# Optimization experiments

Hardware: AMD Instinct MI355X
Metric: run time of the kernel (lower is better)

## Reference

```python
import jax, jax.numpy as jnp
import numpy as np

B, S, H, E, V = 256, 512, 512, 512, 50257
ENC = 2 * H  # bidirectional encoder feature dim
EPS = 1e-40


def setup_inputs() -> dict:
    key = jax.random.key(0)
    ks = jax.random.split(key, 10)
    return {
        "x": jax.random.normal(ks[0], (B, H), jnp.float32),
        "input_embed": jax.random.normal(ks[1], (B, E), jnp.float32),
        "hidden_state": jax.random.normal(ks[2], (B, H), jnp.float32),
        "encoder_output": jax.random.normal(ks[3], (S, B, ENC), jnp.float32),
        "attn_weights": jax.random.uniform(ks[4], (B, S), jnp.float32),
        "input_ids": jax.random.randint(ks[5], (B, S), 0, V, jnp.int64),
        "proj_w": jax.random.normal(ks[6], (V, H), jnp.float32) * (1.0 / np.sqrt(H)),
        "proj_b": jnp.zeros((V,), jnp.float32),
        "pgen_w": jax.random.normal(ks[7], (1, 3 * H + E), jnp.float32) * (1.0 / np.sqrt(3 * H + E)),
        "pgen_b": jnp.zeros((1,), jnp.float32),
    }


def reference(x, input_embed, hidden_state, encoder_output, attn_weights,
              input_ids, proj_w, proj_b, pgen_w, pgen_b):
    temp = 1.0
    # logit: [B, V]
    logit = x @ proj_w.T + proj_b
    # context_state: sum_s attn[b,s] * enc[s,b,:] -> [B, ENC]
    context_state = jnp.einsum("bs,sbh->bh", attn_weights, encoder_output)
    feat = jnp.concatenate([hidden_state, input_embed, context_state], axis=1)
    p_gen = jax.nn.sigmoid(feat @ pgen_w.T + pgen_b)  # [B, 1]
    vocab_dist = jax.nn.softmax(logit / temp, axis=1)
    vocab_dist_ = p_gen * vocab_dist
    p_attn_dist = (1.0 - p_gen) * attn_weights  # [B, S]
    # scatter_add along vocab dim
    rows = jnp.arange(vocab_dist_.shape[0])[:, None]  # [B, 1]
    combined = vocab_dist_.at[rows, input_ids].add(p_attn_dist)
    return jnp.log(combined + EPS)
```

## Files before the change

kernel.cpp:

```cpp
#include <hip/hip_runtime.h>
#include <hip/hip_bf16.h>

#define BB   256
#define SS   512
#define HH   512
#define EE   512
#define VV   50257
#define ENCC 1024
#define NBLK 393
#define VPAD (NBLK * 128)
#define SC   8
#define VT   4096
#define NT   13

typedef __attribute__((ext_vector_type(8))) short short8_t;
typedef __attribute__((ext_vector_type(4))) float f32x4_t;
typedef __attribute__((ext_vector_type(8))) unsigned short ushort8_t;

__device__ __forceinline__ unsigned short f2bf(float f) {
  unsigned u = __builtin_bit_cast(unsigned, f);
  return (unsigned short)((u + 0x7fffu + ((u >> 16) & 1u)) >> 16);
}
__device__ __forceinline__ float bf2f(unsigned short s) {
  return __builtin_bit_cast(float, ((unsigned)s) << 16);
}

__global__ __launch_bounds__(256) void ctx_partial_k(
    const float* __restrict__ attn, const float* __restrict__ enc,
    float* __restrict__ ctxp) {
  const int b = blockIdx.x, sc = blockIdx.y, t = threadIdx.x;
  const int h4 = t * 4;
  const int s0 = sc * (SS / SC);
  const float* ep = enc + (size_t)s0 * BB * ENCC + (size_t)b * ENCC + h4;
  const float* ap = attn + b * SS + s0;
  float4 acc = make_float4(0.f, 0.f, 0.f, 0.f);
#pragma unroll 4
  for (int i = 0; i < SS / SC; ++i) {
    float a = ap[i];
    float4 e = *(const float4*)(ep + (size_t)i * BB * ENCC);
    acc.x += a * e.x; acc.y += a * e.y; acc.z += a * e.z; acc.w += a * e.w;
  }
  *(float4*)(ctxp + ((size_t)(b * SC + sc)) * ENCC + h4) = acc;
}

__global__ __launch_bounds__(256) void pgen_k(
    const float* __restrict__ hidden, const float* __restrict__ embed,
    const float* __restrict__ ctxp, const float* __restrict__ pgw,
    const float* __restrict__ pgb, float* __restrict__ pgen) {
  const int b = blockIdx.x, t = threadIdx.x;
  float acc = 0.f;
  for (int h = t; h < HH; h += 256) acc += hidden[b * HH + h] * pgw[h];
  for (int h = t; h < EE; h += 256) acc += embed[b * EE + h] * pgw[HH + h];
  for (int h = t; h < ENCC; h += 256) {
    float c = 0.f;
#pragma unroll
    for (int p = 0; p < SC; ++p) c += ctxp[((size_t)(b * SC + p)) * ENCC + h];
    acc += c * pgw[HH + EE + h];
  }
#pragma unroll
  for (int off = 32; off; off >>= 1) acc += __shfl_xor(acc, off, 64);
  __shared__ float red[4];
  if ((t & 63) == 0) red[t >> 6] = acc;
  __syncthreads();
  if (t == 0) {
    float s = red[0] + red[1] + red[2] + red[3] + pgb[0];
    pgen[b] = 1.f / (1.f + __expf(-s));
  }
}

__global__ __launch_bounds__(256) void gemm_k(
    const float* __restrict__ x, const float* __restrict__ pw,
    const float* __restrict__ pb, unsigned short* __restrict__ logits,
    float* __restrict__ max_p, float* __restrict__ sum_p) {
  __shared__ unsigned short As[128 * 32];
  __shared__ unsigned short Bs[128 * 32];
  __shared__ float wred[2][128];
  __shared__ float bstat[128];

  const int mb = blockIdx.x, nb = blockIdx.y, t = threadIdx.x;
  const int wave = t >> 6, lane = t & 63;
  const int wm = wave >> 1, wn = wave & 1;
  const int quad = lane >> 4, l16 = lane & 15;
  const int m0 = mb * 128, n0 = nb * 128;
  const int srow = t >> 3, scol = (t & 7) * 4;

  f32x4_t acc[4][4] = {};

  for (int k0 = 0; k0 < HH; k0 += 32) {
    __syncthreads();
#pragma unroll
    for (int i = 0; i < 4; ++i) {
      int r = srow + 32 * i;
      float4 av = *(const float4*)(x + (size_t)(m0 + r) * HH + k0 + scol);
      ushort4 apk;
      apk.x = f2bf(av.x); apk.y = f2bf(av.y); apk.z = f2bf(av.z); apk.w = f2bf(av.w);
      *(ushort4*)&As[r * 32 + scol] = apk;
      int gn = n0 + r;
      float4 bv = make_float4(0.f, 0.f, 0.f, 0.f);
      if (gn < VV) bv = *(const float4*)(pw + (size_t)gn * HH + k0 + scol);
      ushort4 bpk;
      bpk.x = f2bf(bv.x); bpk.y = f2bf(bv.y); bpk.z = f2bf(bv.z); bpk.w = f2bf(bv.w);
      *(ushort4*)&Bs[r * 32 + scol] = bpk;
    }
    __syncthreads();
    short8_t af[4], bf[4];
#pragma unroll
    for (int i = 0; i < 4; ++i) {
      af[i] = *(const short8_t*)&As[(wm * 64 + i * 16 + l16) * 32 + quad * 8];
      bf[i] = *(const short8_t*)&Bs[(wn * 64 + i * 16 + l16) * 32 + quad * 8];
    }
#pragma unroll
    for (int i = 0; i < 4; ++i)
#pragma unroll
      for (int j = 0; j < 4; ++j)
        acc[i][j] = __builtin_amdgcn_mfma_f32_16x16x32_bf16(af[i], bf[j], acc[i][j], 0, 0, 0);
  }

  float bias[4];
  bool okc[4];
#pragma unroll
  for (int j = 0; j < 4; ++j) {
    int col = n0 + wn * 64 + j * 16 + l16;
    okc[j] = (col < VV);
    bias[j] = okc[j] ? pb[col] : 0.f;
  }
#pragma unroll
  for (int i = 0; i < 4; ++i)
#pragma unroll
    for (int j = 0; j < 4; ++j)
#pragma unroll
      for (int r = 0; r < 4; ++r)
        acc[i][j][r] = okc[j] ? (acc[i][j][r] + bias[j]) : -1e30f;

#pragma unroll
  for (int i = 0; i < 4; ++i)
#pragma unroll
    for (int j = 0; j < 4; ++j) {
      int col = n0 + wn * 64 + j * 16 + l16;
      int rowb = wm * 64 + i * 16 + quad * 4;
#pragma unroll
      for (int r = 0; r < 4; ++r)
        logits[(size_t)(m0 + rowb + r) * VPAD + col] = f2bf(acc[i][j][r]);
    }

  float rmax[4][4];
#pragma unroll
  for (int i = 0; i < 4; ++i)
#pragma unroll
    for (int r = 0; r < 4; ++r) {
      float m = fmaxf(fmaxf(acc[i][0][r], acc[i][1][r]), fmaxf(acc[i][2][r], acc[i][3][r]));
#pragma unroll
      for (int off = 1; off < 16; off <<= 1) m = fmaxf(m, __shfl_xor(m, off, 16));
      rmax[i][r] = m;
    }
  if (l16 == 0)
#pragma unroll
    for (int i = 0; i < 4; ++i)
#pragma unroll
      for (int r = 0; r < 4; ++r)
        wred[wn][wm * 64 + i * 16 + quad * 4 + r] = rmax[i][r];
  __syncthreads();
  if (t < 128) bstat[t] = fmaxf(wred[0][t], wred[1][t]);
  __syncthreads();

  float rsum[4][4];
#pragma unroll
  for (int i = 0; i < 4; ++i)
#pragma unroll
    for (int r = 0; r < 4; ++r) {
      float bm = bstat[wm * 64 + i * 16 + quad * 4 + r];
      float s = __expf(acc[i][0][r] - bm) + __expf(acc[i][1][r] - bm)
              + __expf(acc[i][2][r] - bm) + __expf(acc[i][3][r] - bm);
#pragma unroll
      for (int off = 1; off < 16; off <<= 1) s += __shfl_xor(s, off, 16);
      rsum[i][r] = s;
    }
  if (l16 == 0)
#pragma unroll
    for (int i = 0; i < 4; ++i)
#pragma unroll
      for (int r = 0; r < 4; ++r)
        wred[wn][wm * 64 + i * 16 + quad * 4 + r] = rsum[i][r];
  __syncthreads();
  if (t < 128) {
    int rg = m0 + t;
    max_p[rg * NBLK + nb] = bstat[t];
    sum_p[rg * NBLK + nb] = wred[0][t] + wred[1][t];
  }
}

__global__ __launch_bounds__(256) void rowstat_k(
    const float* __restrict__ max_p, const float* __restrict__ sum_p,
    float* __restrict__ row_m, float* __restrict__ row_iz) {
  const int b = blockIdx.x, t = threadIdx.x;
  __shared__ float red[4];
  __shared__ float bmv;
  float m = -1e30f;
  for (int nb = t; nb < NBLK; nb += 256) m = fmaxf(m, max_p[b * NBLK + nb]);
#pragma unroll
  for (int off = 32; off; off >>= 1) m = fmaxf(m, __shfl_xor(m, off, 64));
  if ((t & 63) == 0) red[t >> 6] = m;
  __syncthreads();
  if (t == 0) bmv = fmaxf(fmaxf(red[0], red[1]), fmaxf(red[2], red[3]));
  __syncthreads();
  const float bm = bmv;
  float z = 0.f;
  for (int nb = t; nb < NBLK; nb += 256)
    z += sum_p[b * NBLK + nb] * __expf(max_p[b * NBLK + nb] - bm);
#pragma unroll
  for (int off = 32; off; off >>= 1) z += __shfl_xor(z, off, 64);
  if ((t & 63) == 0) red[t >> 6] = z;
  __syncthreads();
  if (t == 0) {
    row_m[b] = bm;
    row_iz[b] = 1.f / (red[0] + red[1] + red[2] + red[3]);
  }
}

__global__ __launch_bounds__(256) void final_k(
    const unsigned short* __restrict__ logits, const float* __restrict__ row_m,
    const float* __restrict__ row_iz, const float* __restrict__ pgen,
    const float* __restrict__ attn, const int* __restrict__ ids,
    float* __restrict__ out) {
  __shared__ float sl[VT];
  const int vt = blockIdx.x, b = blockIdx.y, t = threadIdx.x;
  const int v0 = vt * VT;
  for (int i = t; i < VT; i += 256) sl[i] = 0.f;
  const float m = row_m[b], iz = row_iz[b], pg = pgen[b];
  const float scale = pg * iz, pa = 1.f - pg;
  __syncthreads();
#pragma unroll
  for (int s = t; s < SS; s += 256) {
    int id = ids[b * SS + s];
    if (id >= v0 && id < v0 + VT) atomicAdd(&sl[id - v0], pa * attn[b * SS + s]);
  }
  float vals[16];
  const unsigned short* lp = logits + (size_t)b * VPAD + v0 + t * 16;
  ushort8_t p0 = *(const ushort8_t*)lp;
  ushort8_t p1 = *(const ushort8_t*)(lp + 8);
#pragma unroll
  for (int j = 0; j < 8; ++j) vals[j] = scale * __expf(bf2f(p0[j]) - m);
#pragma unroll
  for (int j = 0; j < 8; ++j) vals[8 + j] = scale * __expf(bf2f(p1[j]) - m);
  __syncthreads();
  const int vb = v0 + t * 16;
#pragma unroll
  for (int j = 0; j < 16; ++j) {
    int v = vb + j;
    if (v < VV) out[(size_t)b * VV + v] = __logf(vals[j] + sl[t * 16 + j] + 1e-40f);
  }
}

extern "C" void kernel_launch(void* const* d_in, const int* in_sizes, int n_in,
                              void* d_out, int out_size, void* d_ws, size_t ws_size,
                              hipStream_t stream) {
  const float* x      = (const float*)d_in[0];
  const float* embed  = (const float*)d_in[1];
  const float* hidden = (const float*)d_in[2];
  const float* enc    = (const float*)d_in[3];
  const float* attn   = (const float*)d_in[4];
  const int*   ids    = (const int*)d_in[5];
  const float* pw     = (const float*)d_in[6];
  const float* pb     = (const float*)d_in[7];
  const float* pgw    = (const float*)d_in[8];
  const float* pgb    = (const float*)d_in[9];
  float* out = (float*)d_out;

  char* ws = (char*)d_ws;
  unsigned short* logits = (unsigned short*)ws;
  size_t off = (size_t)BB * VPAD * 2;
  float* max_p = (float*)(ws + off); off += (size_t)BB * NBLK * 4;
  float* sum_p = (float*)(ws + off); off += (size_t)BB * NBLK * 4;
  float* ctxp  = (float*)(ws + off); off += (size_t)BB * SC * ENCC * 4;
  float* pgen  = (float*)(ws + off); off += BB * 4;
  float* row_m = (float*)(ws + off); off += BB * 4;
  float* row_iz = (float*)(ws + off);

  ctx_partial_k<<<dim3(BB, SC), 256, 0, stream>>>(attn, enc, ctxp);
  pgen_k<<<dim3(BB), 256, 0, stream>>>(hidden, embed, ctxp, pgw, pgb, pgen);
  gemm_k<<<dim3(2, NBLK), 256, 0, stream>>>(x, pw, pb, logits, max_p, sum_p);
  rowstat_k<<<dim3(BB), 256, 0, stream>>>(max_p, sum_p, row_m, row_iz);
  final_k<<<dim3(NT, BB), 256, 0, stream>>>(logits, row_m, row_iz, pgen, attn, ids, out);
}
```

Measured before the change: 926.8 us.

## Pre-convert x to bf16, widen GEMM tile to all 256 rows, vectorize output stores

Adds a kernel that converts x to bf16 once. The GEMM now uses one 512-thread block per 128-column vocab tile covering all 256 batch rows, so each proj_w tile is loaded and converted once instead of twice. The A tile is staged into LDS with global_load_lds direct copies, and proj_w loads are issued before the barrier. The final kernel computes all 16 logs first and then writes them with float4 stores when in bounds. The trade-off is half as many GEMM blocks (393), which may hurt occupancy, plus an extra launch.

Result: faster. 823.2 us (-11.2%).

```diff
diff --git a/kernel.cpp b/kernel.cpp
--- a/kernel.cpp
+++ b/kernel.cpp
@@ -17,12 +17,24 @@
 typedef __attribute__((ext_vector_type(4))) float f32x4_t;
 typedef __attribute__((ext_vector_type(8))) unsigned short ushort8_t;
 
+typedef __attribute__((address_space(1))) const void gv_t;
+typedef __attribute__((address_space(3))) void lv_t;
+
 __device__ __forceinline__ unsigned short f2bf(float f) {
   unsigned u = __builtin_bit_cast(unsigned, f);
   return (unsigned short)((u + 0x7fffu + ((u >> 16) & 1u)) >> 16);
 }
 __device__ __forceinline__ float bf2f(unsigned short s) {
   return __builtin_bit_cast(float, ((unsigned)s) << 16);
+}
+
+__global__ __launch_bounds__(256) void cvt_x_k(const float* __restrict__ x,
+                                               unsigned short* __restrict__ xbf) {
+  int i = (blockIdx.x * 256 + threadIdx.x) * 4;
+  float4 v = *(const float4*)(x + i);
+  ushort4 p;
+  p.x = f2bf(v.x); p.y = f2bf(v.y); p.z = f2bf(v.z); p.w = f2bf(v.w);
+  *(ushort4*)(xbf + i) = p;
 }
 
 __global__ __launch_bounds__(256) void ctx_partial_k(
@@ -68,40 +80,43 @@
   }
 }
 
-__global__ __launch_bounds__(256) void gemm_k(
-    const float* __restrict__ x, const float* __restrict__ pw,
+__global__ __launch_bounds__(512) void gemm_k(
+    const unsigned short* __restrict__ xbf, const float* __restrict__ pw,
     const float* __restrict__ pb, unsigned short* __restrict__ logits,
     float* __restrict__ max_p, float* __restrict__ sum_p) {
-  __shared__ unsigned short As[128 * 32];
+  __shared__ unsigned short As[256 * 32];
   __shared__ unsigned short Bs[128 * 32];
-  __shared__ float wred[2][128];
-  __shared__ float bstat[128];
-
-  const int mb = blockIdx.x, nb = blockIdx.y, t = threadIdx.x;
+  __shared__ float wred[2][256];
+  __shared__ float bstat[256];
+
+  const int nb = blockIdx.x, t = threadIdx.x;
   const int wave = t >> 6, lane = t & 63;
   const int wm = wave >> 1, wn = wave & 1;
   const int quad = lane >> 4, l16 = lane & 15;
-  const int m0 = mb * 128, n0 = nb * 128;
-  const int srow = t >> 3, scol = (t & 7) * 4;
+  const int n0 = nb * 128;
+  const int br = t >> 2, bc = (t & 3) * 8;
 
   f32x4_t acc[4][4] = {};
 
   for (int k0 = 0; k0 < HH; k0 += 32) {
+    const int gn = n0 + br;
+    float4 b0 = make_float4(0.f, 0.f, 0.f, 0.f), b1 = b0;
+    if (gn < VV) {
+      b0 = *(const float4*)(pw + (size_t)gn * HH + k0 + bc);
+      b1 = *(const float4*)(pw + (size_t)gn * HH + k0 + bc + 4);
+    }
     __syncthreads();
 #pragma unroll
-    for (int i = 0; i < 4; ++i) {
-      int r = srow + 32 * i;
-      float4 av = *(const float4*)(x + (size_t)(m0 + r) * HH + k0 + scol);
-      ushort4 apk;
-      apk.x = f2bf(av.x); apk.y = f2bf(av.y); apk.z = f2bf(av.z); apk.w = f2bf(av.w);
-      *(ushort4*)&As[r * 32 + scol] = apk;
-      int gn = n0 + r;
-      float4 bv = make_float4(0.f, 0.f, 0.f, 0.f);
-      if (gn < VV) bv = *(const float4*)(pw + (size_t)gn * HH + k0 + scol);
-      ushort4 bpk;
-      bpk.x = f2bf(bv.x); bpk.y = f2bf(bv.y); bpk.z = f2bf(bv.z); bpk.w = f2bf(bv.w);
-      *(ushort4*)&Bs[r * 32 + scol] = bpk;
-    }
+    for (int q = 0; q < 2; ++q) {
+      const int c = q * 512 + wave * 64 + lane;
+      const unsigned short* ga = xbf + ((c >> 2) * HH + k0 + (c & 3) * 8);
+      __builtin_amdgcn_global_load_lds((gv_t*)ga, (lv_t*)(As + (size_t)(q * 512 + wave * 64) * 8),
+                                       16, 0, 0);
+    }
+    ushort8_t pk;
+    pk[0] = f2bf(b0.x); pk[1] = f2bf(b0.y); pk[2] = f2bf(b0.z); pk[3] = f2bf(b0.w);
+    pk[4] = f2bf(b1.x); pk[5] = f2bf(b1.y); pk[6] = f2bf(b1.z); pk[7] = f2bf(b1.w);
+    *(ushort8_t*)&Bs[(size_t)t * 8] = pk;
     __syncthreads();
     short8_t af[4], bf[4];
 #pragma unroll
@@ -140,7 +155,7 @@
       int rowb = wm * 64 + i * 16 + quad * 4;
 #pragma unroll
       for (int r = 0; r < 4; ++r)
-        logits[(size_t)(m0 + rowb + r) * VPAD + col] = f2bf(acc[i][j][r]);
+        logits[(size_t)(rowb + r) * VPAD + col] = f2bf(acc[i][j][r]);
     }
 
   float rmax[4][4];
@@ -160,7 +175,7 @@
       for (int r = 0; r < 4; ++r)
         wred[wn][wm * 64 + i * 16 + quad * 4 + r] = rmax[i][r];
   __syncthreads();
-  if (t < 128) bstat[t] = fmaxf(wred[0][t], wred[1][t]);
+  if (t < 256) bstat[t] = fmaxf(wred[0][t], wred[1][t]);
   __syncthreads();
 
   float rsum[4][4];
@@ -182,10 +197,9 @@
       for (int r = 0; r < 4; ++r)
         wred[wn][wm * 64 + i * 16 + quad * 4 + r] = rsum[i][r];
   __syncthreads();
-  if (t < 128) {
-    int rg = m0 + t;
-    max_p[rg * NBLK + nb] = bstat[t];
-    sum_p[rg * NBLK + nb] = wred[0][t] + wred[1][t];
+  if (t < 256) {
+    max_p[t * NBLK + nb] = bstat[t];
+    sum_p[t * NBLK + nb] = wred[0][t] + wred[1][t];
   }
 }
 
@@ -244,10 +258,18 @@
   for (int j = 0; j < 8; ++j) vals[8 + j] = scale * __expf(bf2f(p1[j]) - m);
   __syncthreads();
   const int vb = v0 + t * 16;
-#pragma unroll
-  for (int j = 0; j < 16; ++j) {
-    int v = vb + j;
-    if (v < VV) out[(size_t)b * VV + v] = __logf(vals[j] + sl[t * 16 + j] + 1e-40f);
+  float r[16];
+#pragma unroll
+  for (int j = 0; j < 16; ++j) r[j] = __logf(vals[j] + sl[t * 16 + j] + 1e-40f);
+  if (vb + 15 < VV) {
+    float* op = out + (size_t)b * VV + vb;
+#pragma unroll
+    for (int j = 0; j < 4; ++j)
+      *(float4*)(op + j * 4) = make_float4(r[j * 4], r[j * 4 + 1], r[j * 4 + 2], r[j * 4 + 3]);
+  } else {
+#pragma unroll
+    for (int j = 0; j < 16; ++j)
+      if (vb + j < VV) out[(size_t)b * VV + vb + j] = r[j];
   }
 }
 
@@ -274,11 +296,13 @@
   float* ctxp  = (float*)(ws + off); off += (size_t)BB * SC * ENCC * 4;
   float* pgen  = (float*)(ws + off); off += BB * 4;
   float* row_m = (float*)(ws + off); off += BB * 4;
-  float* row_iz = (float*)(ws + off);
-
+  float* row_iz = (float*)(ws + off); off += BB * 4;
+  unsigned short* xbf = (unsigned short*)(ws + off);
+
+  cvt_x_k<<<dim3((BB * HH) / 1024), 256, 0, stream>>>(x, xbf);
   ctx_partial_k<<<dim3(BB, SC), 256, 0, stream>>>(attn, enc, ctxp);
   pgen_k<<<dim3(BB), 256, 0, stream>>>(hidden, embed, ctxp, pgw, pgb, pgen);
-  gemm_k<<<dim3(2, NBLK), 256, 0, stream>>>(x, pw, pb, logits, max_p, sum_p);
+  gemm_k<<<dim3(NBLK), 512, 0, stream>>>(xbf, pw, pb, logits, max_p, sum_p);
   rowstat_k<<<dim3(BB), 256, 0, stream>>>(max_p, sum_p, row_m, row_iz);
   final_k<<<dim3(NT, BB), 256, 0, stream>>>(logits, row_m, row_iz, pgen, attn, ids, out);
 }
```
